# Kernel tuning notes

Measured on AMD Instinct MI355X. Metric: run time of the kernel, lower is better.

The kernel has to match this reference:

```python
import jax, jax.numpy as jnp
import numpy as np

BATCH, IN_DIM, OUT_DIM = 4096, 8192, 16384

# Each of the 16 logic gates is affine in {1, a, b, a*b}. Rows below give the
# coefficients (const, a, b, ab) for gate k, matching the torch `gate` match-case.
_GATE_COEFS = np.array([
    [0, 0, 0, 0],    # 0: zeros
    [0, 0, 0, 1],    # 1: a*b
    [0, 1, 0, -1],   # 2: a - a*b
    [0, 1, 0, 0],    # 3: a
    [0, 0, 1, -1],   # 4: b - a*b
    [0, 0, 1, 0],    # 5: b
    [0, 1, 1, -2],   # 6: a + b - 2ab (xor)
    [0, 1, 1, -1],   # 7: a + b - ab (or)
    [1, -1, -1, 1],  # 8: 1 - (a + b - ab) (nor)
    [1, -1, -1, 2],  # 9: 1 - (a + b - 2ab) (xnor)
    [1, 0, -1, 0],   # 10: 1 - b
    [1, 0, -1, 1],   # 11: 1 - b + ab
    [1, -1, 0, 0],   # 12: 1 - a
    [1, -1, 0, 1],   # 13: 1 - a + ab
    [1, 0, 0, -1],   # 14: 1 - ab (nand)
    [1, 0, 0, 0],    # 15: ones
], dtype=np.float32)


def setup_inputs() -> dict:
    key = jax.random.key(0)
    k1, k2, k3, k4 = jax.random.split(key, 4)
    x = jax.random.uniform(k1, (BATCH, IN_DIM), dtype=jnp.float32)
    weights = jax.random.normal(k2, (OUT_DIM, 16), dtype=jnp.float32)
    idx_a = jax.random.randint(k3, (OUT_DIM,), 0, IN_DIM, dtype=jnp.int32)
    idx_b = jax.random.randint(k4, (OUT_DIM,), 0, IN_DIM, dtype=jnp.int32)
    return {"x": x, "weights": weights, "idx_a": idx_a, "idx_b": idx_b}


def reference(x, weights, idx_a, idx_b):
    # Training path: softmax over the 16 gate logits per output neuron.
    w = jax.nn.softmax(weights, axis=-1)            # [O, 16]
    # Collapse the 16-gate weighted sum into 4 affine coefficients per neuron.
    coef = w @ jnp.asarray(_GATE_COEFS)             # [O, 4] -> (c0, ca, cb, cab)
    a = x[..., idx_a]                               # [B, O] gather
    b = x[..., idx_b]                               # [B, O] gather
    return coef[:, 0] + coef[:, 1] * a + coef[:, 2] * b + coef[:, 3] * (a * b)
```

## Files before the change

kernel.cpp:

```cpp
#include <hip/hip_runtime.h>
#include <cstddef>
#include <cstdint>

constexpr int BATCH   = 4096;
constexpr int IN_DIM  = 8192;
constexpr int OUT_DIM = 16384;
constexpr int THREADS = 512;
constexpr int RPB     = 2;
constexpr int OPT     = 4;
constexpr int ITERS   = OUT_DIM / (THREADS * OPT);
constexpr int SSTEPS  = IN_DIM / (THREADS * 2);

typedef float f32x2 __attribute__((ext_vector_type(2)));
typedef float f32x4 __attribute__((ext_vector_type(4)));

__device__ __forceinline__ float4 softmax_coef(const float* __restrict__ wrow) {
  const float4* wp = reinterpret_cast<const float4*>(wrow);
  float4 t0 = wp[0], t1 = wp[1], t2 = wp[2], t3 = wp[3];
  float w[16] = { t0.x, t0.y, t0.z, t0.w,
                  t1.x, t1.y, t1.z, t1.w,
                  t2.x, t2.y, t2.z, t2.w,
                  t3.x, t3.y, t3.z, t3.w };
  float m = w[0];
#pragma unroll
  for (int i = 1; i < 16; ++i) m = fmaxf(m, w[i]);
  float p[16];
  float s = 0.f;
#pragma unroll
  for (int i = 0; i < 16; ++i) { p[i] = __expf(w[i] - m); s += p[i]; }
  const float inv = 1.0f / s;
  const float GC[16]  = {0,0,0,0, 0,0,0,0, 1,1,1,1, 1,1,1,1};
  const float GA[16]  = {0,0,1,1, 0,0,1,1, -1,-1,0,0, -1,-1,0,0};
  const float GB[16]  = {0,0,0,0, 1,1,1,1, -1,-1,-1,-1, 0,0,0,0};
  const float GAB[16] = {0,1,-1,0, -1,0,-2,-1, 1,2,0,1, 0,1,-1,0};
  float c0 = 0.f, ca = 0.f, cb = 0.f, cab = 0.f;
#pragma unroll
  for (int i = 0; i < 16; ++i) {
    c0  += p[i] * GC[i];
    ca  += p[i] * GA[i];
    cb  += p[i] * GB[i];
    cab += p[i] * GAB[i];
  }
  return make_float4(c0 * inv, ca * inv, cb * inv, cab * inv);
}

__global__ __launch_bounds__(256)
void coef_kernel(const float* __restrict__ weights, float4* __restrict__ coef) {
  const int o = blockIdx.x * 256 + threadIdx.x;
  if (o < OUT_DIM) coef[o] = softmax_coef(weights + (size_t)o * 16);
}

__global__ __launch_bounds__(THREADS)
void logic_main(const float* __restrict__ x,
                const float4* __restrict__ coef,
                const int* __restrict__ idx_a,
                const int* __restrict__ idx_b,
                float* __restrict__ out) {
  __shared__ float4 xpair[IN_DIM / 2];
  const float2* __restrict__ pr = reinterpret_cast<const float2*>(xpair);

  const int t  = threadIdx.x;
  const int b0 = blockIdx.x * RPB;

  const f32x2* __restrict__ r0 =
      reinterpret_cast<const f32x2*>(x + (size_t)b0 * IN_DIM);
  const f32x2* __restrict__ r1 =
      reinterpret_cast<const f32x2*>(x + (size_t)(b0 + 1) * IN_DIM);

  int o0 = t * OPT;
  int4   ia = *reinterpret_cast<const int4*>(idx_a + o0);
  int4   ib = *reinterpret_cast<const int4*>(idx_b + o0);
  float4 c0 = coef[o0 + 0], c1 = coef[o0 + 1],
         c2 = coef[o0 + 2], c3 = coef[o0 + 3];

#pragma unroll
  for (int s = 0; s < SSTEPS; ++s) {
    const int p = s * THREADS + t;
    f32x2 a = __builtin_nontemporal_load(r0 + p);
    f32x2 b = __builtin_nontemporal_load(r1 + p);
    xpair[p] = make_float4(a.x, b.x, a.y, b.y);
  }
  __syncthreads();

#pragma unroll
  for (int it = 0; it < ITERS; ++it) {
    const int o = it * THREADS * OPT + t * OPT;

    int4 ia_n, ib_n;
    float4 cn0, cn1, cn2, cn3;
    if (it + 1 < ITERS) {
      const int on = o + THREADS * OPT;
      ia_n = *reinterpret_cast<const int4*>(idx_a + on);
      ib_n = *reinterpret_cast<const int4*>(idx_b + on);
      cn0 = coef[on + 0]; cn1 = coef[on + 1];
      cn2 = coef[on + 2]; cn3 = coef[on + 3];
    }

    const float2 A0 = pr[ia.x], A1 = pr[ia.y], A2 = pr[ia.z], A3 = pr[ia.w];
    const float2 B0 = pr[ib.x], B1 = pr[ib.y], B2 = pr[ib.z], B3 = pr[ib.w];

    f32x4 res0, res1;
    res0.x = fmaf(fmaf(c0.w, A0.x, c0.z), B0.x, fmaf(c0.y, A0.x, c0.x));
    res1.x = fmaf(fmaf(c0.w, A0.y, c0.z), B0.y, fmaf(c0.y, A0.y, c0.x));
    res0.y = fmaf(fmaf(c1.w, A1.x, c1.z), B1.x, fmaf(c1.y, A1.x, c1.x));
    res1.y = fmaf(fmaf(c1.w, A1.y, c1.z), B1.y, fmaf(c1.y, A1.y, c1.x));
    res0.z = fmaf(fmaf(c2.w, A2.x, c2.z), B2.x, fmaf(c2.y, A2.x, c2.x));
    res1.z = fmaf(fmaf(c2.w, A2.y, c2.z), B2.y, fmaf(c2.y, A2.y, c2.x));
    res0.w = fmaf(fmaf(c3.w, A3.x, c3.z), B3.x, fmaf(c3.y, A3.x, c3.x));
    res1.w = fmaf(fmaf(c3.w, A3.y, c3.z), B3.y, fmaf(c3.y, A3.y, c3.x));

    __builtin_nontemporal_store(
        res0, reinterpret_cast<f32x4*>(out + (size_t)b0 * OUT_DIM + o));
    __builtin_nontemporal_store(
        res1, reinterpret_cast<f32x4*>(out + (size_t)(b0 + 1) * OUT_DIM + o));

    ia = ia_n; ib = ib_n;
    c0 = cn0; c1 = cn1; c2 = cn2; c3 = cn3;
  }
}

extern "C" void kernel_launch(void* const* d_in, const int* in_sizes, int n_in,
                              void* d_out, int out_size, void* d_ws, size_t ws_size,
                              hipStream_t stream) {
  const float* x       = (const float*)d_in[0];
  const float* weights = (const float*)d_in[1];
  const int*   idx_a   = (const int*)d_in[2];
  const int*   idx_b   = (const int*)d_in[3];
  float*       out     = (float*)d_out;

  float4* coef = (float4*)d_ws;
  coef_kernel<<<OUT_DIM / 256, 256, 0, stream>>>(weights, coef);
  logic_main<<<BATCH / RPB, THREADS, 0, stream>>>(x, coef, idx_a, idx_b, out);
}
```

Measured before the change: 108.9 us.

## Make logic kernel persistent with double-buffered LDS row-pair prefetch

Replaces one block per row pair with 256 persistent 1024-thread blocks, each looping over 8 row pairs. The x rows for the next pair are loaded into registers while the current pair is computed, then written into a second LDS buffer. This is meant to hide global load latency behind the gather and store work and to cut per-block launch and LDS-fill stalls. The cost is 128KB of LDS per block, which allows only one block per CU, plus extra barriers, register pressure from the prefetch arrays, and coef/index loads that are no longer software-prefetched.

```diff
diff --git a/kernel.cpp b/kernel.cpp
--- a/kernel.cpp
+++ b/kernel.cpp
@@ -5,11 +5,12 @@
 constexpr int BATCH   = 4096;
 constexpr int IN_DIM  = 8192;
 constexpr int OUT_DIM = 16384;
-constexpr int THREADS = 512;
-constexpr int RPB     = 2;
+constexpr int THREADS = 1024;
+constexpr int NBLK    = 256;
+constexpr int PAIRS   = (BATCH / 2) / NBLK;
 constexpr int OPT     = 4;
 constexpr int ITERS   = OUT_DIM / (THREADS * OPT);
-constexpr int SSTEPS  = IN_DIM / (THREADS * 2);
+constexpr int SSTEPS  = (IN_DIM / 2) / THREADS;
 
 typedef float f32x2 __attribute__((ext_vector_type(2)));
 typedef float f32x4 __attribute__((ext_vector_type(4)));
@@ -56,66 +57,87 @@
                 const int* __restrict__ idx_a,
                 const int* __restrict__ idx_b,
                 float* __restrict__ out) {
-  __shared__ float4 xpair[IN_DIM / 2];
-  const float2* __restrict__ pr = reinterpret_cast<const float2*>(xpair);
+  __shared__ float4 xpair[2][IN_DIM / 2];
 
-  const int t  = threadIdx.x;
-  const int b0 = blockIdx.x * RPB;
+  const int t    = threadIdx.x;
+  const int row0 = blockIdx.x * (2 * PAIRS);
 
-  const f32x2* __restrict__ r0 =
-      reinterpret_cast<const f32x2*>(x + (size_t)b0 * IN_DIM);
-  const f32x2* __restrict__ r1 =
-      reinterpret_cast<const f32x2*>(x + (size_t)(b0 + 1) * IN_DIM);
+  f32x2 la[SSTEPS], lb[SSTEPS];
 
-  int o0 = t * OPT;
-  int4   ia = *reinterpret_cast<const int4*>(idx_a + o0);
-  int4   ib = *reinterpret_cast<const int4*>(idx_b + o0);
-  float4 c0 = coef[o0 + 0], c1 = coef[o0 + 1],
-         c2 = coef[o0 + 2], c3 = coef[o0 + 3];
-
+  {
+    const f32x2* __restrict__ r0 =
+        reinterpret_cast<const f32x2*>(x + (size_t)row0 * IN_DIM);
+    const f32x2* __restrict__ r1 =
+        reinterpret_cast<const f32x2*>(x + (size_t)(row0 + 1) * IN_DIM);
 #pragma unroll
-  for (int s = 0; s < SSTEPS; ++s) {
-    const int p = s * THREADS + t;
-    f32x2 a = __builtin_nontemporal_load(r0 + p);
-    f32x2 b = __builtin_nontemporal_load(r1 + p);
-    xpair[p] = make_float4(a.x, b.x, a.y, b.y);
+    for (int s = 0; s < SSTEPS; ++s) {
+      const int q = s * THREADS + t;
+      la[s] = __builtin_nontemporal_load(r0 + q);
+      lb[s] = __builtin_nontemporal_load(r1 + q);
+    }
+#pragma unroll
+    for (int s = 0; s < SSTEPS; ++s) {
+      const int q = s * THREADS + t;
+      xpair[0][q] = make_float4(la[s].x, lb[s].x, la[s].y, lb[s].y);
+    }
   }
   __syncthreads();
 
+  for (int p = 0; p < PAIRS; ++p) {
+    const int b0 = row0 + 2 * p;
+    const float2* __restrict__ pr =
+        reinterpret_cast<const float2*>(&xpair[p & 1][0]);
+
+    if (p + 1 < PAIRS) {
+      const f32x2* __restrict__ r0 =
+          reinterpret_cast<const f32x2*>(x + (size_t)(b0 + 2) * IN_DIM);
+      const f32x2* __restrict__ r1 =
+          reinterpret_cast<const f32x2*>(x + (size_t)(b0 + 3) * IN_DIM);
 #pragma unroll
-  for (int it = 0; it < ITERS; ++it) {
-    const int o = it * THREADS * OPT + t * OPT;
-
-    int4 ia_n, ib_n;
-    float4 cn0, cn1, cn2, cn3;
-    if (it + 1 < ITERS) {
-      const int on = o + THREADS * OPT;
-      ia_n = *reinterpret_cast<const int4*>(idx_a + on);
-      ib_n = *reinterpret_cast<const int4*>(idx_b + on);
-      cn0 = coef[on + 0]; cn1 = coef[on + 1];
-      cn2 = coef[on + 2]; cn3 = coef[on + 3];
+      for (int s = 0; s < SSTEPS; ++s) {
+        const int q = s * THREADS + t;
+        la[s] = __builtin_nontemporal_load(r0 + q);
+        lb[s] = __builtin_nontemporal_load(r1 + q);
+      }
     }
 
-    const float2 A0 = pr[ia.x], A1 = pr[ia.y], A2 = pr[ia.z], A3 = pr[ia.w];
-    const float2 B0 = pr[ib.x], B1 = pr[ib.y], B2 = pr[ib.z], B3 = pr[ib.w];
+#pragma unroll
+    for (int it = 0; it < ITERS; ++it) {
+      const int o = it * (THREADS * OPT) + t * OPT;
 
-    f32x4 res0, res1;
-    res0.x = fmaf(fmaf(c0.w, A0.x, c0.z), B0.x, fmaf(c0.y, A0.x, c0.x));
-    res1.x = fmaf(fmaf(c0.w, A0.y, c0.z), B0.y, fmaf(c0.y, A0.y, c0.x));
-    res0.y = fmaf(fmaf(c1.w, A1.x, c1.z), B1.x, fmaf(c1.y, A1.x, c1.x));
-    res1.y = fmaf(fmaf(c1.w, A1.y, c1.z), B1.y, fmaf(c1.y, A1.y, c1.x));
-    res0.z = fmaf(fmaf(c2.w, A2.x, c2.z), B2.x, fmaf(c2.y, A2.x, c2.x));
-    res1.z = fmaf(fmaf(c2.w, A2.y, c2.z), B2.y, fmaf(c2.y, A2.y, c2.x));
-    res0.w = fmaf(fmaf(c3.w, A3.x, c3.z), B3.x, fmaf(c3.y, A3.x, c3.x));
-    res1.w = fmaf(fmaf(c3.w, A3.y, c3.z), B3.y, fmaf(c3.y, A3.y, c3.x));
+      const int4 ia = *reinterpret_cast<const int4*>(idx_a + o);
+      const int4 ib = *reinterpret_cast<const int4*>(idx_b + o);
+      const float4 c0 = coef[o + 0], c1 = coef[o + 1],
+                   c2 = coef[o + 2], c3 = coef[o + 3];
 
-    __builtin_nontemporal_store(
-        res0, reinterpret_cast<f32x4*>(out + (size_t)b0 * OUT_DIM + o));
-    __builtin_nontemporal_store(
-        res1, reinterpret_cast<f32x4*>(out + (size_t)(b0 + 1) * OUT_DIM + o));
+      const float2 A0 = pr[ia.x], A1 = pr[ia.y], A2 = pr[ia.z], A3 = pr[ia.w];
+      const float2 B0 = pr[ib.x], B1 = pr[ib.y], B2 = pr[ib.z], B3 = pr[ib.w];
 
-    ia = ia_n; ib = ib_n;
-    c0 = cn0; c1 = cn1; c2 = cn2; c3 = cn3;
+      f32x4 res0, res1;
+      res0.x = fmaf(fmaf(c0.w, A0.x, c0.z), B0.x, fmaf(c0.y, A0.x, c0.x));
+      res1.x = fmaf(fmaf(c0.w, A0.y, c0.z), B0.y, fmaf(c0.y, A0.y, c0.x));
+      res0.y = fmaf(fmaf(c1.w, A1.x, c1.z), B1.x, fmaf(c1.y, A1.x, c1.x));
+      res1.y = fmaf(fmaf(c1.w, A1.y, c1.z), B1.y, fmaf(c1.y, A1.y, c1.x));
+      res0.z = fmaf(fmaf(c2.w, A2.x, c2.z), B2.x, fmaf(c2.y, A2.x, c2.x));
+      res1.z = fmaf(fmaf(c2.w, A2.y, c2.z), B2.y, fmaf(c2.y, A2.y, c2.x));
+      res0.w = fmaf(fmaf(c3.w, A3.x, c3.z), B3.x, fmaf(c3.y, A3.x, c3.x));
+      res1.w = fmaf(fmaf(c3.w, A3.y, c3.z), B3.y, fmaf(c3.y, A3.y, c3.x));
+
+      __builtin_nontemporal_store(
+          res0, reinterpret_cast<f32x4*>(out + (size_t)b0 * OUT_DIM + o));
+      __builtin_nontemporal_store(
+          res1, reinterpret_cast<f32x4*>(out + (size_t)(b0 + 1) * OUT_DIM + o));
+    }
+    __syncthreads();
+
+    if (p + 1 < PAIRS) {
+#pragma unroll
+      for (int s = 0; s < SSTEPS; ++s) {
+        const int q = s * THREADS + t;
+        xpair[(p + 1) & 1][q] = make_float4(la[s].x, lb[s].x, la[s].y, lb[s].y);
+      }
+      __syncthreads();
+    }
   }
 }
 
@@ -130,5 +152,5 @@
 
   float4* coef = (float4*)d_ws;
   coef_kernel<<<OUT_DIM / 256, 256, 0, stream>>>(weights, coef);
-  logic_main<<<BATCH / RPB, THREADS, 0, stream>>>(x, coef, idx_a, idx_b, out);
+  logic_main<<<NBLK, THREADS, 0, stream>>>(x, coef, idx_a, idx_b, out);
 }
```

Result: slower. 140.8 us (+29.4%).

## Store staged x rows as packed bf16 in LDS and pack gather indices

Applied to the files above, without the earlier changes.

The staged pair of x rows is now held in shared memory as packed bf16 pairs, one 32-bit word per input column, which halves the LDS footprint from 64KB to 32KB so more blocks can reside per CU. The two index arrays are packed into one 16+16-bit word in the coefficient pre-kernel, halving index loads in the main loop. The block size drops to 256 threads and the explicit software prefetch is replaced by a partial unroll. Rounding x to bf16 adds error of roughly 1e-3 relative, which may exceed the checking tolerance.

```diff
diff --git a/kernel.cpp b/kernel.cpp
--- a/kernel.cpp
+++ b/kernel.cpp
@@ -5,27 +5,44 @@
 constexpr int BATCH   = 4096;
 constexpr int IN_DIM  = 8192;
 constexpr int OUT_DIM = 16384;
-constexpr int THREADS = 512;
-constexpr int RPB     = 2;
+constexpr int THREADS = 256;
+constexpr int NBLK    = BATCH / 2;
 constexpr int OPT     = 4;
 constexpr int ITERS   = OUT_DIM / (THREADS * OPT);
-constexpr int SSTEPS  = IN_DIM / (THREADS * 2);
+constexpr int SSTEPS  = (IN_DIM / 2) / THREADS;
 
-typedef float f32x2 __attribute__((ext_vector_type(2)));
-typedef float f32x4 __attribute__((ext_vector_type(4)));
+typedef float    f32x2 __attribute__((ext_vector_type(2)));
+typedef float    f32x4 __attribute__((ext_vector_type(4)));
+typedef uint32_t u32x2 __attribute__((ext_vector_type(2)));
 
-__device__ __forceinline__ float4 softmax_coef(const float* __restrict__ wrow) {
-  const float4* wp = reinterpret_cast<const float4*>(wrow);
+__device__ __forceinline__ uint32_t f2bf(float f) {
+  uint32_t u = __float_as_uint(f);
+  u += 0x7fffu + ((u >> 16) & 1u);
+  return u >> 16;
+}
+__device__ __forceinline__ uint32_t pack_bf(float a, float b) {
+  return f2bf(a) | (f2bf(b) << 16);
+}
+__device__ __forceinline__ float bf_lo(uint32_t u) { return __uint_as_float(u << 16); }
+__device__ __forceinline__ float bf_hi(uint32_t u) { return __uint_as_float(u & 0xffff0000u); }
+
+__global__ __launch_bounds__(256)
+void coef_kernel(const float* __restrict__ weights,
+                 const int* __restrict__ idx_a,
+                 const int* __restrict__ idx_b,
+                 float4* __restrict__ coef,
+                 uint32_t* __restrict__ pidx) {
+  const int o = blockIdx.x * 256 + threadIdx.x;
+  if (o >= OUT_DIM) return;
+
+  const float4* wp = reinterpret_cast<const float4*>(weights + (size_t)o * 16);
   float4 t0 = wp[0], t1 = wp[1], t2 = wp[2], t3 = wp[3];
-  float w[16] = { t0.x, t0.y, t0.z, t0.w,
-                  t1.x, t1.y, t1.z, t1.w,
-                  t2.x, t2.y, t2.z, t2.w,
-                  t3.x, t3.y, t3.z, t3.w };
+  float w[16] = { t0.x, t0.y, t0.z, t0.w, t1.x, t1.y, t1.z, t1.w,
+                  t2.x, t2.y, t2.z, t2.w, t3.x, t3.y, t3.z, t3.w };
   float m = w[0];
 #pragma unroll
   for (int i = 1; i < 16; ++i) m = fmaxf(m, w[i]);
-  float p[16];
-  float s = 0.f;
+  float p[16]; float s = 0.f;
 #pragma unroll
   for (int i = 0; i < 16; ++i) { p[i] = __expf(w[i] - m); s += p[i]; }
   const float inv = 1.0f / s;
@@ -36,86 +53,83 @@
   float c0 = 0.f, ca = 0.f, cb = 0.f, cab = 0.f;
 #pragma unroll
   for (int i = 0; i < 16; ++i) {
-    c0  += p[i] * GC[i];
-    ca  += p[i] * GA[i];
-    cb  += p[i] * GB[i];
-    cab += p[i] * GAB[i];
+    c0 += p[i] * GC[i]; ca += p[i] * GA[i];
+    cb += p[i] * GB[i]; cab += p[i] * GAB[i];
   }
-  return make_float4(c0 * inv, ca * inv, cb * inv, cab * inv);
-}
-
-__global__ __launch_bounds__(256)
-void coef_kernel(const float* __restrict__ weights, float4* __restrict__ coef) {
-  const int o = blockIdx.x * 256 + threadIdx.x;
-  if (o < OUT_DIM) coef[o] = softmax_coef(weights + (size_t)o * 16);
+  coef[o] = make_float4(c0 * inv, ca * inv, cb * inv, cab * inv);
+  pidx[o] = (uint32_t)idx_a[o] | ((uint32_t)idx_b[o] << 16);
 }
 
 __global__ __launch_bounds__(THREADS)
 void logic_main(const float* __restrict__ x,
                 const float4* __restrict__ coef,
-                const int* __restrict__ idx_a,
-                const int* __restrict__ idx_b,
+                const uint32_t* __restrict__ pidx,
                 float* __restrict__ out) {
-  __shared__ float4 xpair[IN_DIM / 2];
-  const float2* __restrict__ pr = reinterpret_cast<const float2*>(xpair);
+  __shared__ uint32_t xp[IN_DIM];
 
   const int t  = threadIdx.x;
-  const int b0 = blockIdx.x * RPB;
+  const int b0 = blockIdx.x * 2;
 
   const f32x2* __restrict__ r0 =
       reinterpret_cast<const f32x2*>(x + (size_t)b0 * IN_DIM);
   const f32x2* __restrict__ r1 =
       reinterpret_cast<const f32x2*>(x + (size_t)(b0 + 1) * IN_DIM);
 
-  int o0 = t * OPT;
-  int4   ia = *reinterpret_cast<const int4*>(idx_a + o0);
-  int4   ib = *reinterpret_cast<const int4*>(idx_b + o0);
-  float4 c0 = coef[o0 + 0], c1 = coef[o0 + 1],
-         c2 = coef[o0 + 2], c3 = coef[o0 + 3];
-
 #pragma unroll
   for (int s = 0; s < SSTEPS; ++s) {
-    const int p = s * THREADS + t;
-    f32x2 a = __builtin_nontemporal_load(r0 + p);
-    f32x2 b = __builtin_nontemporal_load(r1 + p);
-    xpair[p] = make_float4(a.x, b.x, a.y, b.y);
+    const int q = s * THREADS + t;
+    f32x2 a = __builtin_nontemporal_load(r0 + q);
+    f32x2 b = __builtin_nontemporal_load(r1 + q);
+    u32x2 pk;
+    pk.x = pack_bf(a.x, b.x);
+    pk.y = pack_bf(a.y, b.y);
+    *reinterpret_cast<u32x2*>(&xp[2 * q]) = pk;
   }
   __syncthreads();
 
-#pragma unroll
+#pragma unroll 4
   for (int it = 0; it < ITERS; ++it) {
-    const int o = it * THREADS * OPT + t * OPT;
+    const int o = it * (THREADS * OPT) + t * OPT;
 
-    int4 ia_n, ib_n;
-    float4 cn0, cn1, cn2, cn3;
-    if (it + 1 < ITERS) {
-      const int on = o + THREADS * OPT;
-      ia_n = *reinterpret_cast<const int4*>(idx_a + on);
-      ib_n = *reinterpret_cast<const int4*>(idx_b + on);
-      cn0 = coef[on + 0]; cn1 = coef[on + 1];
-      cn2 = coef[on + 2]; cn3 = coef[on + 3];
-    }
+    const int4 pi = *reinterpret_cast<const int4*>(pidx + o);
+    const float4 c0 = coef[o + 0], c1 = coef[o + 1],
+                 c2 = coef[o + 2], c3 = coef[o + 3];
 
-    const float2 A0 = pr[ia.x], A1 = pr[ia.y], A2 = pr[ia.z], A3 = pr[ia.w];
-    const float2 B0 = pr[ib.x], B1 = pr[ib.y], B2 = pr[ib.z], B3 = pr[ib.w];
+    const uint32_t ga0 = xp[(uint32_t)pi.x & 0xffffu], gb0 = xp[(uint32_t)pi.x >> 16];
+    const uint32_t ga1 = xp[(uint32_t)pi.y & 0xffffu], gb1 = xp[(uint32_t)pi.y >> 16];
+    const uint32_t ga2 = xp[(uint32_t)pi.z & 0xffffu], gb2 = xp[(uint32_t)pi.z >> 16];
+    const uint32_t ga3 = xp[(uint32_t)pi.w & 0xffffu], gb3 = xp[(uint32_t)pi.w >> 16];
 
     f32x4 res0, res1;
-    res0.x = fmaf(fmaf(c0.w, A0.x, c0.z), B0.x, fmaf(c0.y, A0.x, c0.x));
-    res1.x = fmaf(fmaf(c0.w, A0.y, c0.z), B0.y, fmaf(c0.y, A0.y, c0.x));
-    res0.y = fmaf(fmaf(c1.w, A1.x, c1.z), B1.x, fmaf(c1.y, A1.x, c1.x));
-    res1.y = fmaf(fmaf(c1.w, A1.y, c1.z), B1.y, fmaf(c1.y, A1.y, c1.x));
-    res0.z = fmaf(fmaf(c2.w, A2.x, c2.z), B2.x, fmaf(c2.y, A2.x, c2.x));
-    res1.z = fmaf(fmaf(c2.w, A2.y, c2.z), B2.y, fmaf(c2.y, A2.y, c2.x));
-    res0.w = fmaf(fmaf(c3.w, A3.x, c3.z), B3.x, fmaf(c3.y, A3.x, c3.x));
-    res1.w = fmaf(fmaf(c3.w, A3.y, c3.z), B3.y, fmaf(c3.y, A3.y, c3.x));
+    {
+      const float a0 = bf_lo(ga0), b0v = bf_lo(gb0);
+      const float a1 = bf_hi(ga0), b1v = bf_hi(gb0);
+      res0.x = fmaf(fmaf(c0.w, a0, c0.z), b0v, fmaf(c0.y, a0, c0.x));
+      res1.x = fmaf(fmaf(c0.w, a1, c0.z), b1v, fmaf(c0.y, a1, c0.x));
+    }
+    {
+      const float a0 = bf_lo(ga1), b0v = bf_lo(gb1);
+      const float a1 = bf_hi(ga1), b1v = bf_hi(gb1);
+      res0.y = fmaf(fmaf(c1.w, a0, c1.z), b0v, fmaf(c1.y, a0, c1.x));
+      res1.y = fmaf(fmaf(c1.w, a1, c1.z), b1v, fmaf(c1.y, a1, c1.x));
+    }
+    {
+      const float a0 = bf_lo(ga2), b0v = bf_lo(gb2);
+      const float a1 = bf_hi(ga2), b1v = bf_hi(gb2);
+      res0.z = fmaf(fmaf(c2.w, a0, c2.z), b0v, fmaf(c2.y, a0, c2.x));
+      res1.z = fmaf(fmaf(c2.w, a1, c2.z), b1v, fmaf(c2.y, a1, c2.x));
+    }
+    {
+      const float a0 = bf_lo(ga3), b0v = bf_lo(gb3);
+      const float a1 = bf_hi(ga3), b1v = bf_hi(gb3);
+      res0.w = fmaf(fmaf(c3.w, a0, c3.z), b0v, fmaf(c3.y, a0, c3.x));
+      res1.w = fmaf(fmaf(c3.w, a1, c3.z), b1v, fmaf(c3.y, a1, c3.x));
+    }
 
     __builtin_nontemporal_store(
         res0, reinterpret_cast<f32x4*>(out + (size_t)b0 * OUT_DIM + o));
     __builtin_nontemporal_store(
         res1, reinterpret_cast<f32x4*>(out + (size_t)(b0 + 1) * OUT_DIM + o));
-
-    ia = ia_n; ib = ib_n;
-    c0 = cn0; c1 = cn1; c2 = cn2; c3 = cn3;
   }
 }
 
@@ -128,7 +142,9 @@
   const int*   idx_b   = (const int*)d_in[3];
   float*       out     = (float*)d_out;
 
-  float4* coef = (float4*)d_ws;
-  coef_kernel<<<OUT_DIM / 256, 256, 0, stream>>>(weights, coef);
-  logic_main<<<BATCH / RPB, THREADS, 0, stream>>>(x, coef, idx_a, idx_b, out);
+  float4*   coef = (float4*)d_ws;
+  uint32_t* pidx = (uint32_t*)((char*)d_ws + (size_t)OUT_DIM * 16);
+
+  coef_kernel<<<OUT_DIM / 256, 256, 0, stream>>>(weights, idx_a, idx_b, coef, pidx);
+  logic_main<<<NBLK, THREADS, 0, stream>>>(x, coef, pidx, out);
 }
```

After: 106.6 us. 2.1% less time.
